# Kernel optimization log

Measured on AMD Instinct MI355X. Metric: run time of the kernel, lower is better.

## Reference

```python
import jax, jax.numpy as jnp
import numpy as np

B, C, D, W, H = 2, 256, 16, 32, 32
CS = 256          # in_channels_style
SN = 256          # number of style tokens
HEADS = 8
DH = C // HEADS
EPS = 1e-6


def setup_inputs() -> dict:
    key = jax.random.key(0)
    ks = jax.random.split(key, 8)
    x = jax.random.normal(ks[0], (B, C, D, W, H), dtype=jnp.float32)
    s = jax.random.normal(ks[1], (B, SN, CS), dtype=jnp.float32)
    # learned parameters
    ln_w = jnp.ones((C,), jnp.float32)
    ln_b = jnp.zeros((C,), jnp.float32)
    lns_w = jnp.ones((CS,), jnp.float32)
    lns_b = jnp.zeros((CS,), jnp.float32)
    sc = 0.02
    Wq = jax.random.normal(ks[2], (C, C), jnp.float32) * sc   # (out, in) 1x1 conv3d
    Wk = jax.random.normal(ks[3], (C, CS), jnp.float32) * sc  # Linear weight (out, in)
    Wv = jax.random.normal(ks[4], (C, CS), jnp.float32) * sc
    Wo = jax.random.normal(ks[5], (C, C), jnp.float32) * sc   # proj_out 1x1 conv3d
    bo = jnp.zeros((C,), jnp.float32)
    return {"x": x, "s": s, "ln_w": ln_w, "ln_b": ln_b, "lns_w": lns_w,
            "lns_b": lns_b, "Wq": Wq, "Wk": Wk, "Wv": Wv, "Wo": Wo, "bo": bo}


def reference(x, s, ln_w, ln_b, lns_w, lns_b, Wq, Wk, Wv, Wo, bo):
    b = x.shape[0]
    # channels_first LayerNorm over channel dim (dim 1) of 5D tensor
    u = x.mean(axis=1, keepdims=True)
    var = ((x - u) ** 2).mean(axis=1, keepdims=True)
    hn = (x - u) / jnp.sqrt(var + EPS)
    hn = ln_w[None, :, None, None, None] * hn + ln_b[None, :, None, None, None]
    # standard LayerNorm on last dim of style tokens
    mu = s.mean(axis=-1, keepdims=True)
    sv = ((s - mu) ** 2).mean(axis=-1, keepdims=True)
    sn = (s - mu) / jnp.sqrt(sv + EPS) * lns_w + lns_b
    # projections: 1x1 conv3d == channel matmul; linears on style
    q = jnp.einsum('bcdwh,oc->bodwh', hn, Wq)               # (B,C,D,W,H)
    k = jnp.einsum('bnc,oc->bon', sn, Wk)                    # (B,C,Sn)
    v = jnp.einsum('bnc,oc->bon', sn, Wv)                    # (B,C,Sn)
    d, w, h = q.shape[2], q.shape[3], q.shape[4]
    N = d * w * h
    q = q.reshape(b * HEADS, DH, N).transpose(0, 2, 1)       # (B*h, N, dh)
    k = k.reshape(b * HEADS, DH, SN)                         # (B*h, dh, Sn)
    v = v.reshape(b * HEADS, DH, SN)                         # (B*h, dh, Sn)
    scores = jnp.einsum('bnd,bds->bns', q, k) * (DH ** -0.5)
    attn = jax.nn.softmax(scores, axis=2)                    # (B*h, N, Sn)
    out = jnp.einsum('bds,bns->bdn', v, attn)                # (B*h, dh, N)
    out = out.reshape(b, C, d, w, h)
    out = jnp.einsum('bcdwh,oc->bodwh', out, Wo) + bo[None, :, None, None, None]
    return x + out
```

## Files before the change

### kernel.cpp

```cpp
#include <hip/hip_runtime.h>

#define EPS_ 1e-6f

typedef __attribute__((ext_vector_type(8))) short bf16x8;
typedef __attribute__((ext_vector_type(4))) float f32x4;

__device__ __forceinline__ unsigned short f2b(float f){
  union { float f; unsigned int u; } v; v.f = f;
  unsigned int r = v.u + 0x7fffu + ((v.u >> 16) & 1u);
  return (unsigned short)(r >> 16);
}
__device__ __forceinline__ unsigned int packrne(float a, float b){
  return (unsigned int)f2b(a) | ((unsigned int)f2b(b) << 16);
}
__device__ __forceinline__ unsigned int packtr(float a, float b){
  return (__float_as_uint(a) >> 16) | (__float_as_uint(b) & 0xffff0000u);
}
union cvt8 { unsigned int u[4]; bf16x8 v; };

__global__ __launch_bounds__(256) void k_prep(
    const float* __restrict__ Wq, const float* __restrict__ Wk,
    const float* __restrict__ Wv, const float* __restrict__ Wo,
    const float* __restrict__ s, const float* __restrict__ lns_w,
    const float* __restrict__ lns_b,
    unsigned short* __restrict__ bWq, unsigned short* __restrict__ bWo,
    unsigned short* __restrict__ Kb, unsigned short* __restrict__ Vb){
  __shared__ unsigned short snb[64*264];
  int t = threadIdx.x;
  int blk = blockIdx.x;
  if (blk < 256){
    int i = blk*256 + t;
    bWq[i] = f2b(Wq[i]);
    bWo[i] = f2b(Wo[i]);
    return;
  }
  int idx = blk - 256;
  int b = idx >> 3, n0 = ((idx >> 1) & 3) * 64, mat = idx & 1;
  int tok = t >> 2, sub = t & 3;
  {
    const float4* srow = (const float4*)(s + ((size_t)(b*256 + n0 + tok))*256 + sub*64);
    float4 vv[16];
    float s1 = 0.f, s2 = 0.f;
    #pragma unroll
    for (int j=0;j<16;++j){
      float4 v = srow[j]; vv[j] = v;
      s1 += (v.x+v.y)+(v.z+v.w);
      s2 += (v.x*v.x+v.y*v.y)+(v.z*v.z+v.w*v.w);
    }
    s1 += __shfl_xor(s1,1); s1 += __shfl_xor(s1,2);
    s2 += __shfl_xor(s2,1); s2 += __shfl_xor(s2,2);
    float mu = s1*(1.f/256.f);
    float rstd = rsqrtf(s2*(1.f/256.f) - mu*mu + EPS_);
    const float4* wr = (const float4*)(lns_w + sub*64);
    const float4* br = (const float4*)(lns_b + sub*64);
    #pragma unroll
    for (int j=0;j<16;++j){
      float4 v = vv[j], g = wr[j], o = br[j];
      float n0v = (v.x-mu)*rstd*g.x + o.x;
      float n1v = (v.y-mu)*rstd*g.y + o.y;
      float n2v = (v.z-mu)*rstd*g.z + o.z;
      float n3v = (v.w-mu)*rstd*g.w + o.w;
      uint2 pk = { packrne(n0v,n1v), packrne(n2v,n3v) };
      *(uint2*)&snb[tok*264 + sub*64 + j*4] = pk;
    }
  }
  __syncthreads();
  int lane = t & 63, w = t >> 6, quad = lane >> 4, l16 = lane & 15;
  const float* W = mat ? Wv : Wk;
  f32x4 acc[4][4];
  #pragma unroll
  for (int ot=0;ot<4;++ot)
    #pragma unroll
    for (int nt=0;nt<4;++nt) acc[ot][nt] = (f32x4){0.f,0.f,0.f,0.f};
  for (int ks=0; ks<8; ++ks){
    bf16x8 afr[4], bfr[4];
    #pragma unroll
    for (int ot=0;ot<4;++ot){
      const float4* wr = (const float4*)(W + (size_t)(w*64 + ot*16 + l16)*256 + ks*32 + quad*8);
      float4 a0 = wr[0], a1 = wr[1];
      cvt8 cv;
      cv.u[0]=packrne(a0.x,a0.y); cv.u[1]=packrne(a0.z,a0.w);
      cv.u[2]=packrne(a1.x,a1.y); cv.u[3]=packrne(a1.z,a1.w);
      afr[ot] = cv.v;
    }
    #pragma unroll
    for (int nt=0;nt<4;++nt)
      bfr[nt] = *(const bf16x8*)&snb[(nt*16+l16)*264 + ks*32 + quad*8];
    #pragma unroll
    for (int ot=0;ot<4;++ot)
      #pragma unroll
      for (int nt=0;nt<4;++nt)
        acc[ot][nt] = __builtin_amdgcn_mfma_f32_16x16x32_bf16(afr[ot], bfr[nt], acc[ot][nt], 0,0,0);
  }
  #pragma unroll
  for (int ot=0;ot<4;++ot){
    int otg = w*4 + ot;
    int h = otg >> 1, dbase = (otg&1)*16 + quad*4;
    #pragma unroll
    for (int nt=0;nt<4;++nt){
      int n = n0 + nt*16 + l16;
      if (!mat){
        uint2 pk = { packrne(acc[ot][nt][0], acc[ot][nt][1]),
                     packrne(acc[ot][nt][2], acc[ot][nt][3]) };
        *(uint2*)&Kb[(((size_t)(b*8+h))*256 + n)*32 + dbase] = pk;
      } else {
        #pragma unroll
        for (int r=0;r<4;++r)
          Vb[(((size_t)(b*8+h))*32 + dbase + r)*256 + n] = f2b(acc[ot][nt][r]);
      }
    }
  }
}

__global__ __launch_bounds__(256,4) void k_mega(
    const float* __restrict__ x, const float* __restrict__ ln_w,
    const float* __restrict__ ln_b,
    const unsigned short* __restrict__ bWq, const unsigned short* __restrict__ bWo,
    const unsigned short* __restrict__ Kb, const unsigned short* __restrict__ Vb,
    const float* __restrict__ bo, float* __restrict__ out){
  __shared__ unsigned short buf1[32*264];
  __shared__ float st[512];
  int t = threadIdx.x;
  int blk = blockIdx.x;
  int b = blk >> 9, p0 = (blk & 511) << 5;

  {
    int p4 = t & 7, cg = t >> 3;
    const float* xq = x + ((size_t)(b*256 + cg*8) << 14) + p0 + p4*4;
    float vr[8][4];
    #pragma unroll
    for (int j=0;j<8;++j){
      float4 v = *(const float4*)(xq + ((size_t)j << 14));
      vr[j][0]=v.x; vr[j][1]=v.y; vr[j][2]=v.z; vr[j][3]=v.w;
    }
    float s1v[4]={0.f,0.f,0.f,0.f}, s2v[4]={0.f,0.f,0.f,0.f};
    #pragma unroll
    for (int j=0;j<8;++j)
      #pragma unroll
      for (int i=0;i<4;++i){ s1v[i]+=vr[j][i]; s2v[i]+=vr[j][i]*vr[j][i]; }
    #pragma unroll
    for (int i=0;i<4;++i){
      s1v[i]+=__shfl_xor(s1v[i],8);  s2v[i]+=__shfl_xor(s2v[i],8);
      s1v[i]+=__shfl_xor(s1v[i],16); s2v[i]+=__shfl_xor(s2v[i],16);
      s1v[i]+=__shfl_xor(s1v[i],32); s2v[i]+=__shfl_xor(s2v[i],32);
    }
    int wv = t >> 6;
    if ((t & 56) == 0){
      #pragma unroll
      for (int i=0;i<4;++i){
        st[(wv*8 + p4)*4 + i]       = s1v[i];
        st[128 + (wv*8 + p4)*4 + i] = s2v[i];
      }
    }
    __syncthreads();
    float mu[4], rstd[4];
    #pragma unroll
    for (int i=0;i<4;++i){
      float a = st[(0*8+p4)*4+i] + st[(1*8+p4)*4+i]
              + st[(2*8+p4)*4+i] + st[(3*8+p4)*4+i];
      float q = st[128+(0*8+p4)*4+i] + st[128+(1*8+p4)*4+i]
              + st[128+(2*8+p4)*4+i] + st[128+(3*8+p4)*4+i];
      mu[i] = a*(1.f/256.f);
      rstd[i] = rsqrtf(q*(1.f/256.f) - mu[i]*mu[i] + EPS_);
    }
    float lwv[8], lbv[8];
    {
      float4 a0 = *(const float4*)(ln_w + cg*8);
      float4 a1 = *(const float4*)(ln_w + cg*8 + 4);
      float4 b0 = *(const float4*)(ln_b + cg*8);
      float4 b1 = *(const float4*)(ln_b + cg*8 + 4);
      lwv[0]=a0.x; lwv[1]=a0.y; lwv[2]=a0.z; lwv[3]=a0.w;
      lwv[4]=a1.x; lwv[5]=a1.y; lwv[6]=a1.z; lwv[7]=a1.w;
      lbv[0]=b0.x; lbv[1]=b0.y; lbv[2]=b0.z; lbv[3]=b0.w;
      lbv[4]=b1.x; lbv[5]=b1.y; lbv[6]=b1.z; lbv[7]=b1.w;
    }
    #pragma unroll
    for (int i=0;i<4;++i){
      int prow = p4*4 + i;
      float n_[8];
      #pragma unroll
      for (int j=0;j<8;++j)
        n_[j] = (vr[j][i]-mu[i])*rstd[i]*lwv[j] + lbv[j];
      uint2 w0 = { packrne(n_[0],n_[1]), packrne(n_[2],n_[3]) };
      uint2 w1 = { packrne(n_[4],n_[5]), packrne(n_[6],n_[7]) };
      *(uint2*)&buf1[prow*264 + cg*8]     = w0;
      *(uint2*)&buf1[prow*264 + cg*8 + 4] = w1;
    }
  }
  __syncthreads();

  int lane = t & 63, w = t >> 6, quad = lane >> 4, l16 = lane & 15;
  int ptile = w & 1, ohalf = w >> 1;
  int prow = ptile*16 + l16;
  const float qs = 0.17677669529663689f * 1.44269504088896341f;

  {
    f32x4 acc[4][2];
    #pragma unroll
    for (int ot=0;ot<4;++ot)
      #pragma unroll
      for (int pt=0;pt<2;++pt) acc[ot][pt] = (f32x4){0.f,0.f,0.f,0.f};
    const unsigned short* wq = bWq + (size_t)(w*64 + l16)*256 + quad*8;
    #pragma unroll 2
    for (int ks=0; ks<8; ++ks){
      bf16x8 bfr[2], afr[4];
      #pragma unroll
      for (int ot=0;ot<4;++ot)
        afr[ot] = *(const bf16x8*)(wq + (size_t)ot*16*256 + ks*32);
      #pragma unroll
      for (int pt=0;pt<2;++pt)
        bfr[pt] = *(const bf16x8*)&buf1[(pt*16+l16)*264 + ks*32 + quad*8];
      #pragma unroll
      for (int ot=0;ot<4;++ot)
        #pragma unroll
        for (int pt=0;pt<2;++pt)
          acc[ot][pt] = __builtin_amdgcn_mfma_f32_16x16x32_bf16(afr[ot], bfr[pt], acc[ot][pt], 0,0,0);
    }
    __syncthreads();
    #pragma unroll
    for (int ot=0;ot<4;++ot){
      int o = w*64 + ot*16 + quad*4;
      #pragma unroll
      for (int pt=0;pt<2;++pt){
        uint2 pk = { packrne(acc[ot][pt][0]*qs, acc[ot][pt][1]*qs),
                     packrne(acc[ot][pt][2]*qs, acc[ot][pt][3]*qs) };
        *(uint2*)&buf1[(pt*16+l16)*264 + o] = pk;
      }
    }
  }
  __syncthreads();

  int srcA = ((( 2*quad   )&3)<<4) + l16;
  int srcB = (((2*quad + 1)&3)<<4) + l16;
  bool hiq = quad >= 2;
  bf16x8 qf[4];
  #pragma unroll
  for (int hh=0;hh<4;++hh)
    qf[hh] = *(const bf16x8*)&buf1[prow*264 + (ohalf*4+hh)*32 + quad*8];

  for (int hh=0; hh<4; ++hh){
    int h = ohalf*4 + hh;
    int bh = b*8 + h;
    const unsigned short* kb = Kb + (size_t)bh*8192 + quad*8;
    const unsigned short* vb = Vb + (size_t)bh*8192 + quad*8;
    f32x4 av[2] = {{0.f,0.f,0.f,0.f},{0.f,0.f,0.f,0.f}};
    float sm0=0.f, sm1=0.f, sm2=0.f, sm3=0.f;
    #pragma unroll 4
    for (int ks=0; ks<8; ++ks){
      bf16x8 kf0 = *(const bf16x8*)(kb + (size_t)((2*ks  )*16+l16)*32);
      bf16x8 kf1 = *(const bf16x8*)(kb + (size_t)((2*ks+1)*16+l16)*32);
      bf16x8 vf0 = *(const bf16x8*)(vb + (size_t)(     l16)*256 + ks*32);
      bf16x8 vf1 = *(const bf16x8*)(vb + (size_t)(16 + l16)*256 + ks*32);
      f32x4 z = {0.f,0.f,0.f,0.f};
      __builtin_amdgcn_s_setprio(1);
      f32x4 s0 = __builtin_amdgcn_mfma_f32_16x16x32_bf16(kf0, qf[hh], z, 0,0,0);
      f32x4 s1 = __builtin_amdgcn_mfma_f32_16x16x32_bf16(kf1, qf[hh], z, 0,0,0);
      __builtin_amdgcn_s_setprio(0);
      float e00 = exp2f(s0[0]), e01 = exp2f(s0[1]);
      float e02 = exp2f(s0[2]), e03 = exp2f(s0[3]);
      float e10 = exp2f(s1[0]), e11 = exp2f(s1[1]);
      float e12 = exp2f(s1[2]), e13 = exp2f(s1[3]);
      sm0 += e00 + e10; sm1 += e01 + e11;
      sm2 += e02 + e12; sm3 += e03 + e13;
      unsigned int p00 = packtr(e00, e01), p01 = packtr(e02, e03);
      unsigned int p10 = packtr(e10, e11), p11 = packtr(e12, e13);
      unsigned int aA0 = (unsigned int)__shfl((int)p00, srcA);
      unsigned int aB0 = (unsigned int)__shfl((int)p10, srcA);
      unsigned int aA1 = (unsigned int)__shfl((int)p01, srcA);
      unsigned int aB1 = (unsigned int)__shfl((int)p11, srcA);
      unsigned int bA0 = (unsigned int)__shfl((int)p00, srcB);
      unsigned int bB0 = (unsigned int)__shfl((int)p10, srcB);
      unsigned int bA1 = (unsigned int)__shfl((int)p01, srcB);
      unsigned int bB1 = (unsigned int)__shfl((int)p11, srcB);
      cvt8 cv;
      cv.u[0] = hiq ? aB0 : aA0;
      cv.u[1] = hiq ? aB1 : aA1;
      cv.u[2] = hiq ? bB0 : bA0;
      cv.u[3] = hiq ? bB1 : bA1;
      bf16x8 pf = cv.v;
      __builtin_amdgcn_s_setprio(1);
      av[0] = __builtin_amdgcn_mfma_f32_16x16x32_bf16(vf0, pf, av[0], 0,0,0);
      av[1] = __builtin_amdgcn_mfma_f32_16x16x32_bf16(vf1, pf, av[1], 0,0,0);
      __builtin_amdgcn_s_setprio(0);
    }
    float sm = (sm0+sm1)+(sm2+sm3);
    sm += __shfl_xor(sm, 16);
    sm += __shfl_xor(sm, 32);
    float inv = 1.f/sm;
    #pragma unroll
    for (int dt=0; dt<2; ++dt){
      uint2 pko = { packrne(av[dt][0]*inv, av[dt][1]*inv),
                    packrne(av[dt][2]*inv, av[dt][3]*inv) };
      *(uint2*)&buf1[prow*264 + h*32 + dt*16 + quad*4] = pko;
    }
  }
  __syncthreads();

  {
    f32x4 oacc[4][2];
    #pragma unroll
    for (int ot=0;ot<4;++ot)
      #pragma unroll
      for (int pt=0;pt<2;++pt) oacc[ot][pt] = (f32x4){0.f,0.f,0.f,0.f};
    const unsigned short* wo = bWo + (size_t)(w*64 + l16)*256 + quad*8;
    #pragma unroll 2
    for (int ks=0; ks<8; ++ks){
      bf16x8 bfr[2], afr[4];
      #pragma unroll
      for (int ot=0;ot<4;++ot)
        afr[ot] = *(const bf16x8*)(wo + (size_t)ot*16*256 + ks*32);
      #pragma unroll
      for (int pt=0;pt<2;++pt)
        bfr[pt] = *(const bf16x8*)&buf1[(pt*16+l16)*264 + ks*32 + quad*8];
      #pragma unroll
      for (int ot=0;ot<4;++ot)
        #pragma unroll
        for (int pt=0;pt<2;++pt)
          oacc[ot][pt] = __builtin_amdgcn_mfma_f32_16x16x32_bf16(afr[ot], bfr[pt], oacc[ot][pt], 0,0,0);
    }
    float xr[4][2][4];
    #pragma unroll
    for (int ot=0;ot<4;++ot){
      int o = w*64 + ot*16 + quad*4;
      #pragma unroll
      for (int pt=0;pt<2;++pt){
        int p = p0 + pt*16 + l16;
        #pragma unroll
        for (int r=0;r<4;++r)
          xr[ot][pt][r] = x[(((size_t)b*256 + o + r) << 14) + p];
      }
    }
    #pragma unroll
    for (int ot=0;ot<4;++ot){
      int o = w*64 + ot*16 + quad*4;
      #pragma unroll
      for (int pt=0;pt<2;++pt){
        int p = p0 + pt*16 + l16;
        #pragma unroll
        for (int r=0;r<4;++r){
          size_t idx = (((size_t)b*256 + o + r) << 14) + p;
          out[idx] = oacc[ot][pt][r] + bo[o+r] + xr[ot][pt][r];
        }
      }
    }
  }
}

extern "C" void kernel_launch(void* const* d_in, const int* in_sizes, int n_in,
                              void* d_out, int out_size, void* d_ws, size_t ws_size,
                              hipStream_t stream) {
  const float* x     = (const float*)d_in[0];
  const float* s     = (const float*)d_in[1];
  const float* ln_w  = (const float*)d_in[2];
  const float* ln_b  = (const float*)d_in[3];
  const float* lns_w = (const float*)d_in[4];
  const float* lns_b = (const float*)d_in[5];
  const float* Wq    = (const float*)d_in[6];
  const float* Wk    = (const float*)d_in[7];
  const float* Wv    = (const float*)d_in[8];
  const float* Wo    = (const float*)d_in[9];
  const float* bo    = (const float*)d_in[10];
  float* out = (float*)d_out;

  unsigned short* bWq = (unsigned short*)d_ws;
  unsigned short* bWo = bWq + 65536;
  unsigned short* Kb  = bWo + 65536;
  unsigned short* Vb  = Kb + 131072;

  k_prep<<<272,  256, 0, stream>>>(Wq, Wk, Wv, Wo, s, lns_w, lns_b, bWq, bWo, Kb, Vb);
  k_mega<<<1024, 256, 0, stream>>>(x, ln_w, ln_b, bWq, bWo, Kb, Vb, bo, out);
}
```

Measured before the change: 188.6 us.

## Switch attention inner loop to 32x32x16 MFMA with per-wave head ownership

Rewrites the fused attention stage so each wave owns two whole heads across all 32 pixel rows and uses 32x32x16 bf16 MFMA for both the score and PV products instead of 16x16x32 tiles. Softmax probabilities are repacked into the B-operand layout with a single xor-32 shuffle pair per half, replacing eight indexed shuffles per step. Because each wave now reads only Q columns it wrote itself, the block barrier between the Q projection and attention is removed. The larger accumulators raise register pressure, and the single accumulator chain serialises the PV MFMAs.

```diff
diff --git a/kernel.cpp b/kernel.cpp
--- a/kernel.cpp
+++ b/kernel.cpp
@@ -4,6 +4,7 @@
 
 typedef __attribute__((ext_vector_type(8))) short bf16x8;
 typedef __attribute__((ext_vector_type(4))) float f32x4;
+typedef __attribute__((ext_vector_type(16))) float f32x16;
 
 __device__ __forceinline__ unsigned short f2b(float f){
   union { float f; unsigned int u; } v; v.f = f;
@@ -190,8 +191,6 @@
   __syncthreads();
 
   int lane = t & 63, w = t >> 6, quad = lane >> 4, l16 = lane & 15;
-  int ptile = w & 1, ohalf = w >> 1;
-  int prow = ptile*16 + l16;
   const float qs = 0.17677669529663689f * 1.44269504088896341f;
 
   {
@@ -228,70 +227,77 @@
       }
     }
   }
-  __syncthreads();
-
-  int srcA = ((( 2*quad   )&3)<<4) + l16;
-  int srcB = (((2*quad + 1)&3)<<4) + l16;
-  bool hiq = quad >= 2;
-  bf16x8 qf[4];
+
+  int r32 = lane & 31;
+  int h5  = lane >> 5;
+  bool hb = h5 != 0;
+
   #pragma unroll
-  for (int hh=0;hh<4;++hh)
-    qf[hh] = *(const bf16x8*)&buf1[prow*264 + (ohalf*4+hh)*32 + quad*8];
-
-  for (int hh=0; hh<4; ++hh){
-    int h = ohalf*4 + hh;
-    int bh = b*8 + h;
-    const unsigned short* kb = Kb + (size_t)bh*8192 + quad*8;
-    const unsigned short* vb = Vb + (size_t)bh*8192 + quad*8;
-    f32x4 av[2] = {{0.f,0.f,0.f,0.f},{0.f,0.f,0.f,0.f}};
-    float sm0=0.f, sm1=0.f, sm2=0.f, sm3=0.f;
-    #pragma unroll 4
-    for (int ks=0; ks<8; ++ks){
-      bf16x8 kf0 = *(const bf16x8*)(kb + (size_t)((2*ks  )*16+l16)*32);
-      bf16x8 kf1 = *(const bf16x8*)(kb + (size_t)((2*ks+1)*16+l16)*32);
-      bf16x8 vf0 = *(const bf16x8*)(vb + (size_t)(     l16)*256 + ks*32);
-      bf16x8 vf1 = *(const bf16x8*)(vb + (size_t)(16 + l16)*256 + ks*32);
-      f32x4 z = {0.f,0.f,0.f,0.f};
+  for (int hh=0; hh<2; ++hh){
+    int head = w*2 + hh;
+    int bh = b*8 + head;
+    const unsigned short* kb = Kb + (size_t)bh*8192 + (size_t)r32*32  + 8*h5;
+    const unsigned short* vb = Vb + (size_t)bh*8192 + (size_t)r32*256 + 8*h5;
+    const unsigned short* qrow = &buf1[r32*264 + head*32 + 8*h5];
+    bf16x8 qf0 = *(const bf16x8*)(qrow);
+    bf16x8 qf1 = *(const bf16x8*)(qrow + 16);
+    f32x16 av;
+    #pragma unroll
+    for (int i=0;i<16;++i) av[i] = 0.f;
+    float sm = 0.f;
+    #pragma unroll 2
+    for (int nc=0; nc<8; ++nc){
+      bf16x8 kf0 = *(const bf16x8*)(kb + nc*1024);
+      bf16x8 kf1 = *(const bf16x8*)(kb + nc*1024 + 16);
+      bf16x8 vf0 = *(const bf16x8*)(vb + nc*32);
+      bf16x8 vf1 = *(const bf16x8*)(vb + nc*32 + 16);
+      f32x16 sc;
+      #pragma unroll
+      for (int i=0;i<16;++i) sc[i] = 0.f;
       __builtin_amdgcn_s_setprio(1);
-      f32x4 s0 = __builtin_amdgcn_mfma_f32_16x16x32_bf16(kf0, qf[hh], z, 0,0,0);
-      f32x4 s1 = __builtin_amdgcn_mfma_f32_16x16x32_bf16(kf1, qf[hh], z, 0,0,0);
+      sc = __builtin_amdgcn_mfma_f32_32x32x16_bf16(kf0, qf0, sc, 0,0,0);
+      sc = __builtin_amdgcn_mfma_f32_32x32x16_bf16(kf1, qf1, sc, 0,0,0);
       __builtin_amdgcn_s_setprio(0);
-      float e00 = exp2f(s0[0]), e01 = exp2f(s0[1]);
-      float e02 = exp2f(s0[2]), e03 = exp2f(s0[3]);
-      float e10 = exp2f(s1[0]), e11 = exp2f(s1[1]);
-      float e12 = exp2f(s1[2]), e13 = exp2f(s1[3]);
-      sm0 += e00 + e10; sm1 += e01 + e11;
-      sm2 += e02 + e12; sm3 += e03 + e13;
-      unsigned int p00 = packtr(e00, e01), p01 = packtr(e02, e03);
-      unsigned int p10 = packtr(e10, e11), p11 = packtr(e12, e13);
-      unsigned int aA0 = (unsigned int)__shfl((int)p00, srcA);
-      unsigned int aB0 = (unsigned int)__shfl((int)p10, srcA);
-      unsigned int aA1 = (unsigned int)__shfl((int)p01, srcA);
-      unsigned int aB1 = (unsigned int)__shfl((int)p11, srcA);
-      unsigned int bA0 = (unsigned int)__shfl((int)p00, srcB);
-      unsigned int bB0 = (unsigned int)__shfl((int)p10, srcB);
-      unsigned int bA1 = (unsigned int)__shfl((int)p01, srcB);
-      unsigned int bB1 = (unsigned int)__shfl((int)p11, srcB);
-      cvt8 cv;
-      cv.u[0] = hiq ? aB0 : aA0;
-      cv.u[1] = hiq ? aB1 : aA1;
-      cv.u[2] = hiq ? bB0 : bA0;
-      cv.u[3] = hiq ? bB1 : bA1;
-      bf16x8 pf = cv.v;
+      float e0 = exp2f(sc[0]), e1 = exp2f(sc[1]), e2 = exp2f(sc[2]), e3 = exp2f(sc[3]);
+      float e4 = exp2f(sc[4]), e5 = exp2f(sc[5]), e6 = exp2f(sc[6]), e7 = exp2f(sc[7]);
+      sm += ((e0+e1)+(e2+e3)) + ((e4+e5)+(e6+e7));
+      unsigned int k0 = packtr(e0,e1), k1 = packtr(e2,e3);
+      unsigned int k2 = packtr(e4,e5), k3 = packtr(e6,e7);
+      unsigned int sA = hb ? k0 : k2, sB = hb ? k1 : k3;
+      unsigned int rA = (unsigned int)__shfl_xor((int)sA, 32);
+      unsigned int rB = (unsigned int)__shfl_xor((int)sB, 32);
+      cvt8 c0;
+      c0.u[0] = hb ? rA : k0;
+      c0.u[1] = hb ? rB : k1;
+      c0.u[2] = hb ? k2 : rA;
+      c0.u[3] = hb ? k3 : rB;
       __builtin_amdgcn_s_setprio(1);
-      av[0] = __builtin_amdgcn_mfma_f32_16x16x32_bf16(vf0, pf, av[0], 0,0,0);
-      av[1] = __builtin_amdgcn_mfma_f32_16x16x32_bf16(vf1, pf, av[1], 0,0,0);
+      av = __builtin_amdgcn_mfma_f32_32x32x16_bf16(vf0, c0.v, av, 0,0,0);
       __builtin_amdgcn_s_setprio(0);
-    }
-    float sm = (sm0+sm1)+(sm2+sm3);
-    sm += __shfl_xor(sm, 16);
+      float e8  = exp2f(sc[8]),  e9  = exp2f(sc[9]),  e10 = exp2f(sc[10]), e11 = exp2f(sc[11]);
+      float e12 = exp2f(sc[12]), e13 = exp2f(sc[13]), e14 = exp2f(sc[14]), e15 = exp2f(sc[15]);
+      sm += ((e8+e9)+(e10+e11)) + ((e12+e13)+(e14+e15));
+      unsigned int k4 = packtr(e8,e9),   k5 = packtr(e10,e11);
+      unsigned int k6 = packtr(e12,e13), k7 = packtr(e14,e15);
+      unsigned int sC = hb ? k4 : k6, sD = hb ? k5 : k7;
+      unsigned int rC = (unsigned int)__shfl_xor((int)sC, 32);
+      unsigned int rD = (unsigned int)__shfl_xor((int)sD, 32);
+      cvt8 c1;
+      c1.u[0] = hb ? rC : k4;
+      c1.u[1] = hb ? rD : k5;
+      c1.u[2] = hb ? k6 : rC;
+      c1.u[3] = hb ? k7 : rD;
+      __builtin_amdgcn_s_setprio(1);
+      av = __builtin_amdgcn_mfma_f32_32x32x16_bf16(vf1, c1.v, av, 0,0,0);
+      __builtin_amdgcn_s_setprio(0);
+    }
     sm += __shfl_xor(sm, 32);
     float inv = 1.f/sm;
     #pragma unroll
-    for (int dt=0; dt<2; ++dt){
-      uint2 pko = { packrne(av[dt][0]*inv, av[dt][1]*inv),
-                    packrne(av[dt][2]*inv, av[dt][3]*inv) };
-      *(uint2*)&buf1[prow*264 + h*32 + dt*16 + quad*4] = pko;
+    for (int g=0; g<4; ++g){
+      uint2 pko = { packrne(av[4*g]*inv,   av[4*g+1]*inv),
+                    packrne(av[4*g+2]*inv, av[4*g+3]*inv) };
+      *(uint2*)&buf1[r32*264 + head*32 + 8*g + 4*h5] = pko;
     }
   }
   __syncthreads();
```

New measurement: 166.9 us. -11.5%, faster.
